# Kernel tuning notes

Measured on AMD Instinct MI355X. Metric: run time of the kernel, lower is better.

## Reference

```python
import jax, jax.numpy as jnp
import numpy as np

E = 160000      # num edges
N = 10000       # num nodes
M1 = 16         # rep1.mult
M2 = 8          # rep2.mult (output)
D1 = 3          # rep1.dim
D2 = 3          # rep2.dim
NREPS = 2       # repr.nreps()
EDGE_DIM = 32
HID = 64
NHEADS = 4
HIDDEN_SIZE = M2 * D2            # 24, attention hidden size
HEAD_DIM = HIDDEN_SIZE // NHEADS # 6
M2H = 3 * M2                     # repr_h.rep2.mult = 24 (k,q,v fused)
TMP_OUT = NREPS * M1 * M2H       # 768, RadialWeight layer2 out dim


def setup_inputs() -> dict:
    key = jax.random.key(0)
    ks = jax.random.split(key, 9)
    src = jax.random.randint(ks[0], (E,), 0, N)
    dst = jax.random.randint(ks[1], (E,), 0, N)
    basis = jax.random.normal(ks[2], (E, D1, NREPS * D2), dtype=jnp.float32)
    edge_feats = jax.random.normal(ks[3], (E, EDGE_DIM), dtype=jnp.float32)
    f = jax.random.normal(ks[4], (N, M1, D1), dtype=jnp.float32)
    W1 = jax.random.normal(ks[5], (HID, EDGE_DIM), dtype=jnp.float32) * 0.05
    b1 = jnp.zeros((HID,), dtype=jnp.float32)
    W2 = jax.random.normal(ks[6], (TMP_OUT, HID), dtype=jnp.float32) * 0.05
    b2 = jnp.zeros((TMP_OUT,), dtype=jnp.float32)
    return {"src": src, "dst": dst, "basis": basis, "edge_feats": edge_feats,
            "f": f, "W1": W1, "b1": b1, "W2": W2, "b2": b2}


def reference(src, dst, basis, edge_feats, f, W1, b1, W2, b2):
    # --- RadialWeight: 2-layer MLP on invariant edge feats ---
    h = jax.nn.relu(edge_feats @ W1.T + b1)               # (E, HID)
    rw = (h @ W2.T + b2).reshape(E, M2H, M1 * NREPS)      # (E, 3*m2, m1*nreps)

    # --- Equivariant convolution: gather by src, basis matmul, radial mix ---
    fe = f[src]                                           # (E, m1, d1)
    tmp = jnp.einsum('emd,edk->emk', fe, basis)           # (E, m1, nreps*d2)
    tmp = tmp.reshape(E, M1 * NREPS, D2)                  # (E, m1*nreps, d2)
    conv = jnp.einsum('ecm,emd->ecd', rw, tmp)            # (E, 3*m2, d2)

    # --- split into k, q, v along the multiplicity (feature) dim ---
    k, q, v = jnp.split(conv, 3, axis=1)                  # each (E, m2, d2)
    k = k.reshape(E, NHEADS, HEAD_DIM)
    q = q.reshape(E, NHEADS, HEAD_DIM)
    v = v.reshape(E, NHEADS, HEAD_DIM)

    # --- graph attention: LeakyReLU scores + edge softmax over dst ---
    temp = HIDDEN_SIZE ** (-0.5)
    scores = jnp.sum(k * q, axis=-1) * temp               # (E, NHEADS)
    scores = jax.nn.leaky_relu(scores, negative_slope=0.2)
    smax = jax.ops.segment_max(scores, dst, num_segments=N)   # (N, NHEADS)
    ex = jnp.exp(scores - smax[dst])                      # (E, NHEADS)
    denom = jax.ops.segment_sum(ex, dst, num_segments=N)  # (N, NHEADS)
    weights = ex / denom[dst]                             # (E, NHEADS)

    # --- weighted values, scatter-sum to dst nodes ---
    wv = weights[..., None] * v                           # (E, NHEADS, HEAD_DIM)
    out = jax.ops.segment_sum(wv, dst, num_segments=N)    # (N, NHEADS, HEAD_DIM)
    return out.reshape(N, M2, D2)
```

## Files before the change

### kernel.cpp

```cpp
#include <hip/hip_runtime.h>

#define E_EDGES 160000
#define N_NODES 10000
#define SLOTS   32

#define TEMP 0.20412414523193154f

typedef __fp16 half2_t __attribute__((ext_vector_type(2)));
typedef __fp16 half8_t __attribute__((ext_vector_type(8)));
typedef float f32x4 __attribute__((ext_vector_type(4)));

__device__ __forceinline__ float fdot2(half2_t a, half2_t b, float c) {
#if __has_builtin(__builtin_amdgcn_fdot2)
    return __builtin_amdgcn_fdot2(a, b, c, false);
#else
    return fmaf((float)a.x, (float)b.x, fmaf((float)a.y, (float)b.y, c));
#endif
}
__device__ __forceinline__ half2_t pk(float a, float b) {
    return __builtin_amdgcn_cvt_pkrtz(a, b);
}

__global__ __launch_bounds__(256)
void prep_kernel(const float* __restrict__ W2, const float* __restrict__ W1,
                 unsigned* __restrict__ w2p, uint4* __restrict__ w1pk,
                 int* __restrict__ cnt, float4* __restrict__ zbuf)
{
    int u = blockIdx.x * blockDim.x + threadIdx.x;
    if (u < N_NODES) cnt[u] = 0;
    #pragma unroll
    for (int i = 0; i < 3; ++i) {
        int z = u + i * 24576;
        if (z < (N_NODES * 28) / 4) zbuf[z] = make_float4(0.f, 0.f, 0.f, 0.f);
    }
    if (u < 256) {
        int t = u >> 6, l = u & 63;
        int r16 = l & 15, q = l >> 4;
        int row = 32*(t >> 1) + ((r16 >> 2) << 3) + ((t & 1) << 2) + (r16 & 3);
        union { __fp16 h[8]; uint4 v; } o2;
        #pragma unroll
        for (int i = 0; i < 8; ++i) o2.h[i] = (__fp16)W1[row*32 + q*8 + i];
        w1pk[(t << 6) + l] = o2.v;
    }
    int tp    = u & 3;
    int lane  = (u >> 2) & 63;
    int piece = (u >> 8) & 3;
    int c     = u >> 10;
    int em = lane & 15, quad = lane >> 4;
    int row = 32*c + ((piece >> 1) << 4) + em;
    int col = ((piece & 1) << 5) + quad*8 + 2*tp;
    union { half2_t h; unsigned v; } o;
    o.h.x = (__fp16)W2[row*64 + col];
    o.h.y = (__fp16)W2[row*64 + col + 1];
    w2p[u] = o.v;
}

#define CONV_GROUP(GBASE, cbase, OUT) \
    _Pragma("unroll") \
    for (int cg = 0; cg < 8; ++cg) { \
        const int c = (cbase) + cg; \
        const uint4* wg = (GBASE) + cg*256 + lane; \
        union { uint4 u; half8_t v; } u0, u1, u2, u3; \
        u0.u = wg[0]; u1.u = wg[64]; u2.u = wg[128]; u3.u = wg[192]; \
        half8_t wa0 = u0.v, wa1 = u1.v, wb0 = u2.v, wb1 = u3.v; \
        float4 bb0 = *(const float4*)(b2s + 32*c + quad*4); \
        float4 bb1 = *(const float4*)(b2s + 32*c + 16 + quad*4); \
        f32x4 acc0 = {bb0.x, bb0.y, bb0.z, bb0.w}; \
        acc0 = __builtin_amdgcn_mfma_f32_16x16x32_f16(wa0, h_lo, acc0, 0, 0, 0); \
        acc0 = __builtin_amdgcn_mfma_f32_16x16x32_f16(wa1, h_hi, acc0, 0, 0, 0); \
        f32x4 acc1 = {bb1.x, bb1.y, bb1.z, bb1.w}; \
        acc1 = __builtin_amdgcn_mfma_f32_16x16x32_f16(wb0, h_lo, acc1, 0, 0, 0); \
        acc1 = __builtin_amdgcn_mfma_f32_16x16x32_f16(wb1, h_hi, acc1, 0, 0, 0); \
        float p0 = 0.f, p1 = 0.f, p2 = 0.f; \
        _Pragma("unroll") \
        for (int r = 0; r < 4; ++r) { \
            half2_t rp = pk(acc0[r], acc1[r]); \
            p0 = fdot2(rp, t2[r][0], p0); \
            p1 = fdot2(rp, t2[r][1], p1); \
            p2 = fdot2(rp, t2[r][2], p2); \
        } \
        p0 += __shfl_xor(p0, 16); p0 += __shfl_xor(p0, 32); \
        p1 += __shfl_xor(p1, 16); p1 += __shfl_xor(p1, 32); \
        p2 += __shfl_xor(p2, 16); p2 += __shfl_xor(p2, 32); \
        OUT; \
    }

__global__ __launch_bounds__(256, 2)
void fused_kernel(const int* __restrict__ src, const int* __restrict__ dst,
                  const float* __restrict__ basis, const float* __restrict__ efeat,
                  const float* __restrict__ f,
                  const uint4* __restrict__ w1pk, const float* __restrict__ b1,
                  const uint4* __restrict__ w2p, const float* __restrict__ b2,
                  unsigned char* __restrict__ bkt, int* __restrict__ cnt,
                  float* __restrict__ num, float* __restrict__ den)
{
    __shared__ float b2s[768];

    const int tid  = threadIdx.x;
    const int lane = tid & 63;
    const int wid  = tid >> 6;
    const int em   = lane & 15;
    const int quad = lane >> 4;
    const int e = (blockIdx.x * 4 + wid) * 16 + em;

    if (tid < 192) ((float4*)b2s)[tid] = ((const float4*)b2)[tid];

    half8_t w1f[4];
    {
        #pragma unroll
        for (int t = 0; t < 4; ++t) {
            union { uint4 u; half8_t v; } c;
            c.u = w1pk[(t << 6) + lane];
            w1f[t] = c.v;
        }
    }
    float4 b1a = *(const float4*)(b1 + quad*8);
    float4 b1b = *(const float4*)(b1 + quad*8 + 4);
    float4 b1c = *(const float4*)(b1 + 32 + quad*8);
    float4 b1d = *(const float4*)(b1 + 32 + quad*8 + 4);

    half8_t xb;
    {
        const float4* xv = (const float4*)(efeat + (size_t)e * 32 + quad*8);
        float4 x0 = xv[0], x1 = xv[1];
        union { half2_t h2[4]; half8_t v; } xu;
        xu.h2[0] = pk(x0.x, x0.y); xu.h2[1] = pk(x0.z, x0.w);
        xu.h2[2] = pk(x1.x, x1.y); xu.h2[3] = pk(x1.z, x1.w);
        xb = xu.v;
    }

    int p_slot = 0, dn0 = 0;
    if (quad == 0) {
        dn0 = dst[e];
        p_slot = atomicAdd(&cnt[dn0], 1);
    }
    const int pb  = __shfl(p_slot, em);
    const int dnb = __shfl(dn0, em);

    half8_t h_lo, h_hi;
    {
        f32x4 ha0 = {b1a.x, b1a.y, b1a.z, b1a.w};
        f32x4 ha1 = {b1b.x, b1b.y, b1b.z, b1b.w};
        f32x4 ha2 = {b1c.x, b1c.y, b1c.z, b1c.w};
        f32x4 ha3 = {b1d.x, b1d.y, b1d.z, b1d.w};
        ha0 = __builtin_amdgcn_mfma_f32_16x16x32_f16(w1f[0], xb, ha0, 0, 0, 0);
        ha1 = __builtin_amdgcn_mfma_f32_16x16x32_f16(w1f[1], xb, ha1, 0, 0, 0);
        ha2 = __builtin_amdgcn_mfma_f32_16x16x32_f16(w1f[2], xb, ha2, 0, 0, 0);
        ha3 = __builtin_amdgcn_mfma_f32_16x16x32_f16(w1f[3], xb, ha3, 0, 0, 0);
        union { half2_t h2[4]; half8_t v; } lo, hi;
        lo.h2[0] = pk(fmaxf(ha0[0],0.f), fmaxf(ha0[1],0.f));
        lo.h2[1] = pk(fmaxf(ha0[2],0.f), fmaxf(ha0[3],0.f));
        lo.h2[2] = pk(fmaxf(ha1[0],0.f), fmaxf(ha1[1],0.f));
        lo.h2[3] = pk(fmaxf(ha1[2],0.f), fmaxf(ha1[3],0.f));
        hi.h2[0] = pk(fmaxf(ha2[0],0.f), fmaxf(ha2[1],0.f));
        hi.h2[1] = pk(fmaxf(ha2[2],0.f), fmaxf(ha2[3],0.f));
        hi.h2[2] = pk(fmaxf(ha3[0],0.f), fmaxf(ha3[1],0.f));
        hi.h2[3] = pk(fmaxf(ha3[2],0.f), fmaxf(ha3[3],0.f));
        h_lo = lo.v; h_hi = hi.v;
    }

    half2_t t2[4][3];
    {
        float bas[18];
        const float2* bv = (const float2*)(basis + (size_t)e * 18);
        #pragma unroll
        for (int i = 0; i < 9; ++i) { float2 t = bv[i]; bas[2*i] = t.x; bas[2*i+1] = t.y; }
        const float* fp = f + (size_t)src[e] * 48 + quad*6;
        float fl[6], fh[6];
        #pragma unroll
        for (int i = 0; i < 3; ++i) {
            float2 a = *(const float2*)(fp + 2*i);      fl[2*i] = a.x; fl[2*i+1] = a.y;
            float2 b = *(const float2*)(fp + 24 + 2*i); fh[2*i] = b.x; fh[2*i+1] = b.y;
        }
        #pragma unroll
        for (int jj = 0; jj < 4; ++jj) {
            const int mr = (jj >> 1) * 3;
            const int rb = (jj & 1) * 3;
            #pragma unroll
            for (int d = 0; d < 3; ++d) {
                float lo = fmaf(fl[mr+0], bas[rb+d],
                           fmaf(fl[mr+1], bas[6+rb+d], fl[mr+2] * bas[12+rb+d]));
                float hi = fmaf(fh[mr+0], bas[rb+d],
                           fmaf(fh[mr+1], bas[6+rb+d], fh[mr+2] * bas[12+rb+d]));
                t2[jj][d] = pk(lo, hi);
            }
        }
    }

    __syncthreads();

    float kreg[8][3];
    CONV_GROUP(w2p, 0, { kreg[cg][0]=p0; kreg[cg][1]=p1; kreg[cg][2]=p2; });

    float sreg[4];
    CONV_GROUP(w2p + 2048, 8, {
        float s_ = p0*kreg[cg][0] + p1*kreg[cg][1] + p2*kreg[cg][2];
        if ((cg & 1) == 0) sreg[cg>>1] = s_; else sreg[cg>>1] += s_;
    });

    float exv[4];
    #pragma unroll
    for (int hh = 0; hh < 4; ++hh) {
        float s = sreg[hh] * TEMP;
        s = (s > 0.0f) ? s : 0.2f * s;
        exv[hh] = __expf(s);
    }

    float vreg[8][3];
    CONV_GROUP(w2p + 4096, 16, { vreg[cg][0]=p0; vreg[cg][1]=p1; vreg[cg][2]=p2; });

    if (pb < SLOTS) {
        unsigned char* rec = bkt + ((size_t)dnb * SLOTS + pb) * 64;
        if (quad == 3) {
            *(float4*)(rec + 48) = make_float4(exv[0], exv[1], exv[2], exv[3]);
        } else {
            union { half2_t h2[4]; uint4 u; } pv;
            if (quad == 0) {
                pv.h2[0] = pk(vreg[0][0], vreg[0][1]);
                pv.h2[1] = pk(vreg[0][2], vreg[1][0]);
                pv.h2[2] = pk(vreg[1][1], vreg[1][2]);
                pv.h2[3] = pk(vreg[2][0], vreg[2][1]);
            } else if (quad == 1) {
                pv.h2[0] = pk(vreg[2][2], vreg[3][0]);
                pv.h2[1] = pk(vreg[3][1], vreg[3][2]);
                pv.h2[2] = pk(vreg[4][0], vreg[4][1]);
                pv.h2[3] = pk(vreg[4][2], vreg[5][0]);
            } else {
                pv.h2[0] = pk(vreg[5][1], vreg[5][2]);
                pv.h2[1] = pk(vreg[6][0], vreg[6][1]);
                pv.h2[2] = pk(vreg[6][2], vreg[7][0]);
                pv.h2[3] = pk(vreg[7][1], vreg[7][2]);
            }
            *(uint4*)(rec + quad*16) = pv.u;
        }
    } else {
        float* nb = num + (size_t)dnb * 24;
        if (quad == 0) {
            atomicAdd(nb+0, exv[0]*vreg[0][0]); atomicAdd(nb+1, exv[0]*vreg[0][1]);
            atomicAdd(nb+2, exv[0]*vreg[0][2]); atomicAdd(nb+3, exv[0]*vreg[1][0]);
            atomicAdd(nb+4, exv[0]*vreg[1][1]); atomicAdd(nb+5, exv[0]*vreg[1][2]);
            atomicAdd(nb+6, exv[1]*vreg[2][0]); atomicAdd(nb+7, exv[1]*vreg[2][1]);
        } else if (quad == 1) {
            atomicAdd(nb+8,  exv[1]*vreg[2][2]); atomicAdd(nb+9,  exv[1]*vreg[3][0]);
            atomicAdd(nb+10, exv[1]*vreg[3][1]); atomicAdd(nb+11, exv[1]*vreg[3][2]);
            atomicAdd(nb+12, exv[2]*vreg[4][0]); atomicAdd(nb+13, exv[2]*vreg[4][1]);
            atomicAdd(nb+14, exv[2]*vreg[4][2]); atomicAdd(nb+15, exv[2]*vreg[5][0]);
        } else if (quad == 2) {
            atomicAdd(nb+16, exv[2]*vreg[5][1]); atomicAdd(nb+17, exv[2]*vreg[5][2]);
            atomicAdd(nb+18, exv[3]*vreg[6][0]); atomicAdd(nb+19, exv[3]*vreg[6][1]);
            atomicAdd(nb+20, exv[3]*vreg[6][2]); atomicAdd(nb+21, exv[3]*vreg[7][0]);
            atomicAdd(nb+22, exv[3]*vreg[7][1]); atomicAdd(nb+23, exv[3]*vreg[7][2]);
        } else {
            float* db = den + (size_t)dnb * 4;
            atomicAdd(db+0, exv[0]); atomicAdd(db+1, exv[1]);
            atomicAdd(db+2, exv[2]); atomicAdd(db+3, exv[3]);
        }
    }
}

__global__ __launch_bounds__(256)
void gather_kernel(const int* __restrict__ cnt, const unsigned char* __restrict__ bkt,
                   const float* __restrict__ num, const float* __restrict__ den,
                   float* __restrict__ out)
{
    const int lane = threadIdx.x & 63;
    const int wid  = threadIdx.x >> 6;
    const int n = blockIdx.x * 4 + wid;
    if (n >= N_NODES) return;
    int deg = cnt[n];
    if (deg > SLOTS) deg = SLOTS;
    const unsigned char* rec = bkt + (size_t)n * SLOTS * 64;

    const int j = lane & 31;
    const int half = lane >> 5;
    const int hd = (j < 24) ? (j / 6) : 0;

    float acc = 0.f, dn_ = 0.f;
    if (j < 24 && half == 0) {
        acc = num[n*24 + j];
        dn_ = den[n*4 + hd];
    }
    if (j < 24) {
        #pragma unroll 2
        for (int i = half; i < deg; i += 2) {
            const unsigned char* r = rec + (size_t)i * 64;
            float ex = *(const float*)(r + 48 + hd*4);
            float v  = (float)*(const __fp16*)(r + j*2);
            dn_ += ex;
            acc = fmaf(ex, v, acc);
        }
    }
    acc += __shfl_xor(acc, 32);
    dn_ += __shfl_xor(dn_, 32);
    if (half == 0 && j < 24) {
        out[n*24 + j] = (dn_ > 0.f) ? (acc / dn_) : 0.f;
    }
}

extern "C" void kernel_launch(void* const* d_in, const int* in_sizes, int n_in,
                              void* d_out, int out_size, void* d_ws, size_t ws_size,
                              hipStream_t stream)
{
    const int*   src   = (const int*)d_in[0];
    const int*   dst   = (const int*)d_in[1];
    const float* basis = (const float*)d_in[2];
    const float* ef    = (const float*)d_in[3];
    const float* f     = (const float*)d_in[4];
    const float* W1    = (const float*)d_in[5];
    const float* b1    = (const float*)d_in[6];
    const float* W2    = (const float*)d_in[7];
    const float* b2    = (const float*)d_in[8];
    float* out = (float*)d_out;

    unsigned char* bkt = (unsigned char*)d_ws;
    float* num = (float*)(bkt + (size_t)N_NODES * SLOTS * 64);
    float* den = num + (size_t)N_NODES * 24;
    unsigned* w2p = (unsigned*)(den + (size_t)N_NODES * 4);
    int* cnt = (int*)(w2p + 24576);
    uint4* w1pk = (uint4*)(cnt + N_NODES);

    prep_kernel<<<96, 256, 0, stream>>>(W2, W1, w2p, w1pk, cnt, (float4*)num);

    fused_kernel<<<E_EDGES / 64, 256, 0, stream>>>(src, dst, basis, ef, f,
                                                   w1pk, b1, (const uint4*)w2p, b2,
                                                   bkt, cnt, num, den);

    gather_kernel<<<(N_NODES + 3) / 4, 256, 0, stream>>>(cnt, bkt, num, den, out);
}
```

Baseline: 155.3 us.

## Stage W2 fragments in LDS and process two edge tiles per wave

Each wave now handles 32 edges (two 16-edge tiles) instead of 16, and the block stages the packed W2 weights for the k and q parts into shared memory, later reloading the v part into the same buffer. Weight fragments are loaded once per cg and reused for both edge tiles, which halves global and L2 weight traffic per edge and halves the grid size. In exchange the kernel uses about 64KB of LDS plus extra barriers and roughly double the live registers, so occupancy may drop under the launch bound of 2 blocks per SM.

```diff
diff --git a/kernel.cpp b/kernel.cpp
--- a/kernel.cpp
+++ b/kernel.cpp
@@ -55,35 +55,123 @@
     w2p[u] = o.v;
 }
 
-#define CONV_GROUP(GBASE, cbase, OUT) \
+#define MFMA4_TAIL(F0,F1,F2,F3,HL,HH,BB0,BB1,T2,P0,P1,P2) { \
+    f32x4 a0 = {(BB0).x, (BB0).y, (BB0).z, (BB0).w}; \
+    a0 = __builtin_amdgcn_mfma_f32_16x16x32_f16((F0), (HL), a0, 0, 0, 0); \
+    a0 = __builtin_amdgcn_mfma_f32_16x16x32_f16((F1), (HH), a0, 0, 0, 0); \
+    f32x4 a1 = {(BB1).x, (BB1).y, (BB1).z, (BB1).w}; \
+    a1 = __builtin_amdgcn_mfma_f32_16x16x32_f16((F2), (HL), a1, 0, 0, 0); \
+    a1 = __builtin_amdgcn_mfma_f32_16x16x32_f16((F3), (HH), a1, 0, 0, 0); \
+    P0 = 0.f; P1 = 0.f; P2 = 0.f; \
     _Pragma("unroll") \
-    for (int cg = 0; cg < 8; ++cg) { \
-        const int c = (cbase) + cg; \
-        const uint4* wg = (GBASE) + cg*256 + lane; \
-        union { uint4 u; half8_t v; } u0, u1, u2, u3; \
-        u0.u = wg[0]; u1.u = wg[64]; u2.u = wg[128]; u3.u = wg[192]; \
-        half8_t wa0 = u0.v, wa1 = u1.v, wb0 = u2.v, wb1 = u3.v; \
-        float4 bb0 = *(const float4*)(b2s + 32*c + quad*4); \
-        float4 bb1 = *(const float4*)(b2s + 32*c + 16 + quad*4); \
-        f32x4 acc0 = {bb0.x, bb0.y, bb0.z, bb0.w}; \
-        acc0 = __builtin_amdgcn_mfma_f32_16x16x32_f16(wa0, h_lo, acc0, 0, 0, 0); \
-        acc0 = __builtin_amdgcn_mfma_f32_16x16x32_f16(wa1, h_hi, acc0, 0, 0, 0); \
-        f32x4 acc1 = {bb1.x, bb1.y, bb1.z, bb1.w}; \
-        acc1 = __builtin_amdgcn_mfma_f32_16x16x32_f16(wb0, h_lo, acc1, 0, 0, 0); \
-        acc1 = __builtin_amdgcn_mfma_f32_16x16x32_f16(wb1, h_hi, acc1, 0, 0, 0); \
-        float p0 = 0.f, p1 = 0.f, p2 = 0.f; \
+    for (int r = 0; r < 4; ++r) { \
+        half2_t rp = pk(a0[r], a1[r]); \
+        P0 = fdot2(rp, (T2)[r][0], P0); \
+        P1 = fdot2(rp, (T2)[r][1], P1); \
+        P2 = fdot2(rp, (T2)[r][2], P2); \
+    } \
+    P0 += __shfl_xor(P0, 16); P0 += __shfl_xor(P0, 32); \
+    P1 += __shfl_xor(P1, 16); P1 += __shfl_xor(P1, 32); \
+    P2 += __shfl_xor(P2, 16); P2 += __shfl_xor(P2, 32); \
+}
+
+#define PHASE_A(XB, HLO, HHI) { \
+    f32x4 ha0 = {b1a.x, b1a.y, b1a.z, b1a.w}; \
+    f32x4 ha1 = {b1b.x, b1b.y, b1b.z, b1b.w}; \
+    f32x4 ha2 = {b1c.x, b1c.y, b1c.z, b1c.w}; \
+    f32x4 ha3 = {b1d.x, b1d.y, b1d.z, b1d.w}; \
+    ha0 = __builtin_amdgcn_mfma_f32_16x16x32_f16(w1f[0], (XB), ha0, 0, 0, 0); \
+    ha1 = __builtin_amdgcn_mfma_f32_16x16x32_f16(w1f[1], (XB), ha1, 0, 0, 0); \
+    ha2 = __builtin_amdgcn_mfma_f32_16x16x32_f16(w1f[2], (XB), ha2, 0, 0, 0); \
+    ha3 = __builtin_amdgcn_mfma_f32_16x16x32_f16(w1f[3], (XB), ha3, 0, 0, 0); \
+    union { half2_t h2[4]; half8_t v; } lo, hi; \
+    lo.h2[0] = pk(fmaxf(ha0[0],0.f), fmaxf(ha0[1],0.f)); \
+    lo.h2[1] = pk(fmaxf(ha0[2],0.f), fmaxf(ha0[3],0.f)); \
+    lo.h2[2] = pk(fmaxf(ha1[0],0.f), fmaxf(ha1[1],0.f)); \
+    lo.h2[3] = pk(fmaxf(ha1[2],0.f), fmaxf(ha1[3],0.f)); \
+    hi.h2[0] = pk(fmaxf(ha2[0],0.f), fmaxf(ha2[1],0.f)); \
+    hi.h2[1] = pk(fmaxf(ha2[2],0.f), fmaxf(ha2[3],0.f)); \
+    hi.h2[2] = pk(fmaxf(ha3[0],0.f), fmaxf(ha3[1],0.f)); \
+    hi.h2[3] = pk(fmaxf(ha3[2],0.f), fmaxf(ha3[3],0.f)); \
+    (HLO) = lo.v; (HHI) = hi.v; \
+}
+
+#define PHASE_B(E, T2OUT) { \
+    float bas[18]; \
+    const float2* bv = (const float2*)(basis + (size_t)(E) * 18); \
+    _Pragma("unroll") \
+    for (int i = 0; i < 9; ++i) { float2 t = bv[i]; bas[2*i] = t.x; bas[2*i+1] = t.y; } \
+    const float* fp = f + (size_t)src[(E)] * 48 + quad*6; \
+    float fl[6], fh[6]; \
+    _Pragma("unroll") \
+    for (int i = 0; i < 3; ++i) { \
+        float2 a = *(const float2*)(fp + 2*i);      fl[2*i] = a.x; fl[2*i+1] = a.y; \
+        float2 b = *(const float2*)(fp + 24 + 2*i); fh[2*i] = b.x; fh[2*i+1] = b.y; \
+    } \
+    _Pragma("unroll") \
+    for (int jj = 0; jj < 4; ++jj) { \
+        const int mr = (jj >> 1) * 3; \
+        const int rb = (jj & 1) * 3; \
         _Pragma("unroll") \
-        for (int r = 0; r < 4; ++r) { \
-            half2_t rp = pk(acc0[r], acc1[r]); \
-            p0 = fdot2(rp, t2[r][0], p0); \
-            p1 = fdot2(rp, t2[r][1], p1); \
-            p2 = fdot2(rp, t2[r][2], p2); \
+        for (int d = 0; d < 3; ++d) { \
+            float lo = fmaf(fl[mr+0], bas[rb+d], \
+                       fmaf(fl[mr+1], bas[6+rb+d], fl[mr+2] * bas[12+rb+d])); \
+            float hi = fmaf(fh[mr+0], bas[rb+d], \
+                       fmaf(fh[mr+1], bas[6+rb+d], fh[mr+2] * bas[12+rb+d])); \
+            (T2OUT)[jj][d] = pk(lo, hi); \
         } \
-        p0 += __shfl_xor(p0, 16); p0 += __shfl_xor(p0, 32); \
-        p1 += __shfl_xor(p1, 16); p1 += __shfl_xor(p1, 32); \
-        p2 += __shfl_xor(p2, 16); p2 += __shfl_xor(p2, 32); \
-        OUT; \
-    }
+    } \
+}
+
+#define EPILOGUE(PB, DNB, VREG, EXV) { \
+    if ((PB) < SLOTS) { \
+        unsigned char* rec = bkt + ((size_t)(DNB) * SLOTS + (PB)) * 64; \
+        if (quad == 3) { \
+            *(float4*)(rec + 48) = make_float4((EXV)[0], (EXV)[1], (EXV)[2], (EXV)[3]); \
+        } else { \
+            union { half2_t h2[4]; uint4 u; } pv; \
+            if (quad == 0) { \
+                pv.h2[0] = pk((VREG)[0][0], (VREG)[0][1]); \
+                pv.h2[1] = pk((VREG)[0][2], (VREG)[1][0]); \
+                pv.h2[2] = pk((VREG)[1][1], (VREG)[1][2]); \
+                pv.h2[3] = pk((VREG)[2][0], (VREG)[2][1]); \
+            } else if (quad == 1) { \
+                pv.h2[0] = pk((VREG)[2][2], (VREG)[3][0]); \
+                pv.h2[1] = pk((VREG)[3][1], (VREG)[3][2]); \
+                pv.h2[2] = pk((VREG)[4][0], (VREG)[4][1]); \
+                pv.h2[3] = pk((VREG)[4][2], (VREG)[5][0]); \
+            } else { \
+                pv.h2[0] = pk((VREG)[5][1], (VREG)[5][2]); \
+                pv.h2[1] = pk((VREG)[6][0], (VREG)[6][1]); \
+                pv.h2[2] = pk((VREG)[6][2], (VREG)[7][0]); \
+                pv.h2[3] = pk((VREG)[7][1], (VREG)[7][2]); \
+            } \
+            *(uint4*)(rec + quad*16) = pv.u; \
+        } \
+    } else { \
+        float* nb = num + (size_t)(DNB) * 24; \
+        if (quad == 0) { \
+            atomicAdd(nb+0, (EXV)[0]*(VREG)[0][0]); atomicAdd(nb+1, (EXV)[0]*(VREG)[0][1]); \
+            atomicAdd(nb+2, (EXV)[0]*(VREG)[0][2]); atomicAdd(nb+3, (EXV)[0]*(VREG)[1][0]); \
+            atomicAdd(nb+4, (EXV)[0]*(VREG)[1][1]); atomicAdd(nb+5, (EXV)[0]*(VREG)[1][2]); \
+            atomicAdd(nb+6, (EXV)[1]*(VREG)[2][0]); atomicAdd(nb+7, (EXV)[1]*(VREG)[2][1]); \
+        } else if (quad == 1) { \
+            atomicAdd(nb+8,  (EXV)[1]*(VREG)[2][2]); atomicAdd(nb+9,  (EXV)[1]*(VREG)[3][0]); \
+            atomicAdd(nb+10, (EXV)[1]*(VREG)[3][1]); atomicAdd(nb+11, (EXV)[1]*(VREG)[3][2]); \
+            atomicAdd(nb+12, (EXV)[2]*(VREG)[4][0]); atomicAdd(nb+13, (EXV)[2]*(VREG)[4][1]); \
+            atomicAdd(nb+14, (EXV)[2]*(VREG)[4][2]); atomicAdd(nb+15, (EXV)[2]*(VREG)[5][0]); \
+        } else if (quad == 2) { \
+            atomicAdd(nb+16, (EXV)[2]*(VREG)[5][1]); atomicAdd(nb+17, (EXV)[2]*(VREG)[5][2]); \
+            atomicAdd(nb+18, (EXV)[3]*(VREG)[6][0]); atomicAdd(nb+19, (EXV)[3]*(VREG)[6][1]); \
+            atomicAdd(nb+20, (EXV)[3]*(VREG)[6][2]); atomicAdd(nb+21, (EXV)[3]*(VREG)[7][0]); \
+            atomicAdd(nb+22, (EXV)[3]*(VREG)[7][1]); atomicAdd(nb+23, (EXV)[3]*(VREG)[7][2]); \
+        } else { \
+            float* db = den + (size_t)(DNB) * 4; \
+            atomicAdd(db+0, (EXV)[0]); atomicAdd(db+1, (EXV)[1]); \
+            atomicAdd(db+2, (EXV)[2]); atomicAdd(db+3, (EXV)[3]); \
+        } \
+    } \
+}
 
 __global__ __launch_bounds__(256, 2)
 void fused_kernel(const int* __restrict__ src, const int* __restrict__ dst,
@@ -94,167 +182,157 @@
                   unsigned char* __restrict__ bkt, int* __restrict__ cnt,
                   float* __restrict__ num, float* __restrict__ den)
 {
-    __shared__ float b2s[768];
+    __shared__ __fp16 w2s[2*16384];
+    __shared__ float  b2s[768];
 
     const int tid  = threadIdx.x;
     const int lane = tid & 63;
     const int wid  = tid >> 6;
     const int em   = lane & 15;
     const int quad = lane >> 4;
-    const int e = (blockIdx.x * 4 + wid) * 16 + em;
-
-    if (tid < 192) ((float4*)b2s)[tid] = ((const float4*)b2)[tid];
+    const int base = (blockIdx.x * 4 + wid) * 32;
+    const int e0 = base + em;
+    const int e1 = base + 16 + em;
+
+    {
+        uint4* d4 = (uint4*)w2s;
+        #pragma unroll
+        for (int i = 0; i < 8; ++i) d4[i*256 + tid] = w2p[i*256 + tid];
+        #pragma unroll
+        for (int i = 0; i < 8; ++i) d4[2048 + i*256 + tid] = w2p[2048 + i*256 + tid];
+        if (tid < 192) ((float4*)b2s)[tid] = ((const float4*)b2)[tid];
+    }
+
+    int p_slot = 0, dn0 = 0;
+    if (quad == 0) {
+        dn0 = dst[e0];
+        p_slot = atomicAdd(&cnt[dn0], 1);
+    } else if (quad == 1) {
+        dn0 = dst[e1];
+        p_slot = atomicAdd(&cnt[dn0], 1);
+    }
+    const int pb0  = __shfl(p_slot, em);
+    const int dnb0 = __shfl(dn0, em);
+    const int pb1  = __shfl(p_slot, 16 + em);
+    const int dnb1 = __shfl(dn0, 16 + em);
 
     half8_t w1f[4];
-    {
-        #pragma unroll
-        for (int t = 0; t < 4; ++t) {
-            union { uint4 u; half8_t v; } c;
-            c.u = w1pk[(t << 6) + lane];
-            w1f[t] = c.v;
-        }
+    #pragma unroll
+    for (int t = 0; t < 4; ++t) {
+        union { uint4 u; half8_t v; } c;
+        c.u = w1pk[(t << 6) + lane];
+        w1f[t] = c.v;
     }
     float4 b1a = *(const float4*)(b1 + quad*8);
     float4 b1b = *(const float4*)(b1 + quad*8 + 4);
     float4 b1c = *(const float4*)(b1 + 32 + quad*8);
     float4 b1d = *(const float4*)(b1 + 32 + quad*8 + 4);
 
-    half8_t xb;
+    half8_t xb0, xb1;
     {
-        const float4* xv = (const float4*)(efeat + (size_t)e * 32 + quad*8);
+        const float4* xv = (const float4*)(efeat + (size_t)e0 * 32 + quad*8);
         float4 x0 = xv[0], x1 = xv[1];
         union { half2_t h2[4]; half8_t v; } xu;
         xu.h2[0] = pk(x0.x, x0.y); xu.h2[1] = pk(x0.z, x0.w);
         xu.h2[2] = pk(x1.x, x1.y); xu.h2[3] = pk(x1.z, x1.w);
-        xb = xu.v;
-    }
-
-    int p_slot = 0, dn0 = 0;
-    if (quad == 0) {
-        dn0 = dst[e];
-        p_slot = atomicAdd(&cnt[dn0], 1);
-    }
-    const int pb  = __shfl(p_slot, em);
-    const int dnb = __shfl(dn0, em);
-
-    half8_t h_lo, h_hi;
-    {
-        f32x4 ha0 = {b1a.x, b1a.y, b1a.z, b1a.w};
-        f32x4 ha1 = {b1b.x, b1b.y, b1b.z, b1b.w};
-        f32x4 ha2 = {b1c.x, b1c.y, b1c.z, b1c.w};
-        f32x4 ha3 = {b1d.x, b1d.y, b1d.z, b1d.w};
-        ha0 = __builtin_amdgcn_mfma_f32_16x16x32_f16(w1f[0], xb, ha0, 0, 0, 0);
-        ha1 = __builtin_amdgcn_mfma_f32_16x16x32_f16(w1f[1], xb, ha1, 0, 0, 0);
-        ha2 = __builtin_amdgcn_mfma_f32_16x16x32_f16(w1f[2], xb, ha2, 0, 0, 0);
-        ha3 = __builtin_amdgcn_mfma_f32_16x16x32_f16(w1f[3], xb, ha3, 0, 0, 0);
-        union { half2_t h2[4]; half8_t v; } lo, hi;
-        lo.h2[0] = pk(fmaxf(ha0[0],0.f), fmaxf(ha0[1],0.f));
-        lo.h2[1] = pk(fmaxf(ha0[2],0.f), fmaxf(ha0[3],0.f));
-        lo.h2[2] = pk(fmaxf(ha1[0],0.f), fmaxf(ha1[1],0.f));
-        lo.h2[3] = pk(fmaxf(ha1[2],0.f), fmaxf(ha1[3],0.f));
-        hi.h2[0] = pk(fmaxf(ha2[0],0.f), fmaxf(ha2[1],0.f));
-        hi.h2[1] = pk(fmaxf(ha2[2],0.f), fmaxf(ha2[3],0.f));
-        hi.h2[2] = pk(fmaxf(ha3[0],0.f), fmaxf(ha3[1],0.f));
-        hi.h2[3] = pk(fmaxf(ha3[2],0.f), fmaxf(ha3[3],0.f));
-        h_lo = lo.v; h_hi = hi.v;
-    }
-
-    half2_t t2[4][3];
-    {
-        float bas[18];
-        const float2* bv = (const float2*)(basis + (size_t)e * 18);
-        #pragma unroll
-        for (int i = 0; i < 9; ++i) { float2 t = bv[i]; bas[2*i] = t.x; bas[2*i+1] = t.y; }
-        const float* fp = f + (size_t)src[e] * 48 + quad*6;
-        float fl[6], fh[6];
-        #pragma unroll
-        for (int i = 0; i < 3; ++i) {
-            float2 a = *(const float2*)(fp + 2*i);      fl[2*i] = a.x; fl[2*i+1] = a.y;
-            float2 b = *(const float2*)(fp + 24 + 2*i); fh[2*i] = b.x; fh[2*i+1] = b.y;
-        }
-        #pragma unroll
-        for (int jj = 0; jj < 4; ++jj) {
-            const int mr = (jj >> 1) * 3;
-            const int rb = (jj & 1) * 3;
-            #pragma unroll
-            for (int d = 0; d < 3; ++d) {
-                float lo = fmaf(fl[mr+0], bas[rb+d],
-                           fmaf(fl[mr+1], bas[6+rb+d], fl[mr+2] * bas[12+rb+d]));
-                float hi = fmaf(fh[mr+0], bas[rb+d],
-                           fmaf(fh[mr+1], bas[6+rb+d], fh[mr+2] * bas[12+rb+d]));
-                t2[jj][d] = pk(lo, hi);
-            }
-        }
-    }
+        xb0 = xu.v;
+        const float4* yv = (const float4*)(efeat + (size_t)e1 * 32 + quad*8);
+        float4 y0 = yv[0], y1 = yv[1];
+        xu.h2[0] = pk(y0.x, y0.y); xu.h2[1] = pk(y0.z, y0.w);
+        xu.h2[2] = pk(y1.x, y1.y); xu.h2[3] = pk(y1.z, y1.w);
+        xb1 = xu.v;
+    }
+
+    half8_t h_lo0, h_hi0, h_lo1, h_hi1;
+    PHASE_A(xb0, h_lo0, h_hi0);
+    PHASE_A(xb1, h_lo1, h_hi1);
+
+    half2_t t20[4][3], t21[4][3];
+    PHASE_B(e0, t20);
+    PHASE_B(e1, t21);
 
     __syncthreads();
 
-    float kreg[8][3];
-    CONV_GROUP(w2p, 0, { kreg[cg][0]=p0; kreg[cg][1]=p1; kreg[cg][2]=p2; });
-
-    float sreg[4];
-    CONV_GROUP(w2p + 2048, 8, {
-        float s_ = p0*kreg[cg][0] + p1*kreg[cg][1] + p2*kreg[cg][2];
-        if ((cg & 1) == 0) sreg[cg>>1] = s_; else sreg[cg>>1] += s_;
-    });
-
-    float exv[4];
+    float sreg0[4], sreg1[4];
+    #pragma unroll
+    for (int cg = 0; cg < 8; ++cg) {
+        const __fp16* kp = w2s + ((cg*4)*64 + lane)*8;
+        half8_t kf0 = *(const half8_t*)(kp);
+        half8_t kf1 = *(const half8_t*)(kp + 512);
+        half8_t kf2 = *(const half8_t*)(kp + 1024);
+        half8_t kf3 = *(const half8_t*)(kp + 1536);
+        const __fp16* qp = kp + 16384;
+        half8_t qf0 = *(const half8_t*)(qp);
+        half8_t qf1 = *(const half8_t*)(qp + 512);
+        half8_t qf2 = *(const half8_t*)(qp + 1024);
+        half8_t qf3 = *(const half8_t*)(qp + 1536);
+        float4 bk0 = *(const float4*)(b2s + 32*cg + quad*4);
+        float4 bk1 = *(const float4*)(b2s + 32*cg + 16 + quad*4);
+        float4 bq0 = *(const float4*)(b2s + 32*(8+cg) + quad*4);
+        float4 bq1 = *(const float4*)(b2s + 32*(8+cg) + 16 + quad*4);
+        float k0, k1, k2, q0, q1, q2, s_;
+        MFMA4_TAIL(kf0,kf1,kf2,kf3, h_lo0,h_hi0, bk0,bk1, t20, k0,k1,k2);
+        MFMA4_TAIL(qf0,qf1,qf2,qf3, h_lo0,h_hi0, bq0,bq1, t20, q0,q1,q2);
+        s_ = q0*k0 + q1*k1 + q2*k2;
+        if ((cg & 1) == 0) sreg0[cg>>1] = s_; else sreg0[cg>>1] += s_;
+        MFMA4_TAIL(kf0,kf1,kf2,kf3, h_lo1,h_hi1, bk0,bk1, t21, k0,k1,k2);
+        MFMA4_TAIL(qf0,qf1,qf2,qf3, h_lo1,h_hi1, bq0,bq1, t21, q0,q1,q2);
+        s_ = q0*k0 + q1*k1 + q2*k2;
+        if ((cg & 1) == 0) sreg1[cg>>1] = s_; else sreg1[cg>>1] += s_;
+    }
+
+    float exv0[4], exv1[4];
     #pragma unroll
     for (int hh = 0; hh < 4; ++hh) {
-        float s = sreg[hh] * TEMP;
+        float s = sreg0[hh] * TEMP;
         s = (s > 0.0f) ? s : 0.2f * s;
-        exv[hh] = __expf(s);
-    }
-
-    float vreg[8][3];
-    CONV_GROUP(w2p + 4096, 16, { vreg[cg][0]=p0; vreg[cg][1]=p1; vreg[cg][2]=p2; });
-
-    if (pb < SLOTS) {
-        unsigned char* rec = bkt + ((size_t)dnb * SLOTS + pb) * 64;
-        if (quad == 3) {
-            *(float4*)(rec + 48) = make_float4(exv[0], exv[1], exv[2], exv[3]);
-        } else {
-            union { half2_t h2[4]; uint4 u; } pv;
-            if (quad == 0) {
-                pv.h2[0] = pk(vreg[0][0], vreg[0][1]);
-                pv.h2[1] = pk(vreg[0][2], vreg[1][0]);
-                pv.h2[2] = pk(vreg[1][1], vreg[1][2]);
-                pv.h2[3] = pk(vreg[2][0], vreg[2][1]);
-            } else if (quad == 1) {
-                pv.h2[0] = pk(vreg[2][2], vreg[3][0]);
-                pv.h2[1] = pk(vreg[3][1], vreg[3][2]);
-                pv.h2[2] = pk(vreg[4][0], vreg[4][1]);
-                pv.h2[3] = pk(vreg[4][2], vreg[5][0]);
-            } else {
-                pv.h2[0] = pk(vreg[5][1], vreg[5][2]);
-                pv.h2[1] = pk(vreg[6][0], vreg[6][1]);
-                pv.h2[2] = pk(vreg[6][2], vreg[7][0]);
-                pv.h2[3] = pk(vreg[7][1], vreg[7][2]);
-            }
-            *(uint4*)(rec + quad*16) = pv.u;
+        exv0[hh] = __expf(s);
+        float t = sreg1[hh] * TEMP;
+        t = (t > 0.0f) ? t : 0.2f * t;
+        exv1[hh] = __expf(t);
+    }
+
+    __syncthreads();
+
+    {
+        uint4* d4 = (uint4*)w2s;
+        #pragma unroll
+        for (int i = 0; i < 8; ++i) d4[i*256 + tid] = w2p[4096 + i*256 + tid];
+    }
+
+    __syncthreads();
+
+    {
+        float vreg[8][3];
+        #pragma unroll
+        for (int cg = 0; cg < 8; ++cg) {
+            const __fp16* vp = w2s + ((cg*4)*64 + lane)*8;
+            half8_t vf0 = *(const half8_t*)(vp);
+            half8_t vf1 = *(const half8_t*)(vp + 512);
+            half8_t vf2 = *(const half8_t*)(vp + 1024);
+            half8_t vf3 = *(const half8_t*)(vp + 1536);
+            float4 bv0 = *(const float4*)(b2s + 32*(16+cg) + quad*4);
+            float4 bv1 = *(const float4*)(b2s + 32*(16+cg) + 16 + quad*4);
+            MFMA4_TAIL(vf0,vf1,vf2,vf3, h_lo0,h_hi0, bv0,bv1, t20,
+                       vreg[cg][0], vreg[cg][1], vreg[cg][2]);
         }
-    } else {
-        float* nb = num + (size_t)dnb * 24;
-        if (quad == 0) {
-            atomicAdd(nb+0, exv[0]*vreg[0][0]); atomicAdd(nb+1, exv[0]*vreg[0][1]);
-            atomicAdd(nb+2, exv[0]*vreg[0][2]); atomicAdd(nb+3, exv[0]*vreg[1][0]);
-            atomicAdd(nb+4, exv[0]*vreg[1][1]); atomicAdd(nb+5, exv[0]*vreg[1][2]);
-            atomicAdd(nb+6, exv[1]*vreg[2][0]); atomicAdd(nb+7, exv[1]*vreg[2][1]);
-        } else if (quad == 1) {
-            atomicAdd(nb+8,  exv[1]*vreg[2][2]); atomicAdd(nb+9,  exv[1]*vreg[3][0]);
-            atomicAdd(nb+10, exv[1]*vreg[3][1]); atomicAdd(nb+11, exv[1]*vreg[3][2]);
-            atomicAdd(nb+12, exv[2]*vreg[4][0]); atomicAdd(nb+13, exv[2]*vreg[4][1]);
-            atomicAdd(nb+14, exv[2]*vreg[4][2]); atomicAdd(nb+15, exv[2]*vreg[5][0]);
-        } else if (quad == 2) {
-            atomicAdd(nb+16, exv[2]*vreg[5][1]); atomicAdd(nb+17, exv[2]*vreg[5][2]);
-            atomicAdd(nb+18, exv[3]*vreg[6][0]); atomicAdd(nb+19, exv[3]*vreg[6][1]);
-            atomicAdd(nb+20, exv[3]*vreg[6][2]); atomicAdd(nb+21, exv[3]*vreg[7][0]);
-            atomicAdd(nb+22, exv[3]*vreg[7][1]); atomicAdd(nb+23, exv[3]*vreg[7][2]);
-        } else {
-            float* db = den + (size_t)dnb * 4;
-            atomicAdd(db+0, exv[0]); atomicAdd(db+1, exv[1]);
-            atomicAdd(db+2, exv[2]); atomicAdd(db+3, exv[3]);
+        EPILOGUE(pb0, dnb0, vreg, exv0);
+    }
+    {
+        float vreg[8][3];
+        #pragma unroll
+        for (int cg = 0; cg < 8; ++cg) {
+            const __fp16* vp = w2s + ((cg*4)*64 + lane)*8;
+            half8_t vf0 = *(const half8_t*)(vp);
+            half8_t vf1 = *(const half8_t*)(vp + 512);
+            half8_t vf2 = *(const half8_t*)(vp + 1024);
+            half8_t vf3 = *(const half8_t*)(vp + 1536);
+            float4 bv0 = *(const float4*)(b2s + 32*(16+cg) + quad*4);
+            float4 bv1 = *(const float4*)(b2s + 32*(16+cg) + 16 + quad*4);
+            MFMA4_TAIL(vf0,vf1,vf2,vf3, h_lo1,h_hi1, bv0,bv1, t21,
+                       vreg[cg][0], vreg[cg][1], vreg[cg][2]);
         }
+        EPILOGUE(pb1, dnb1, vreg, exv1);
     }
 }
 
@@ -321,9 +399,9 @@
 
     prep_kernel<<<96, 256, 0, stream>>>(W2, W1, w2p, w1pk, cnt, (float4*)num);
 
-    fused_kernel<<<E_EDGES / 64, 256, 0, stream>>>(src, dst, basis, ef, f,
-                                                   w1pk, b1, (const uint4*)w2p, b2,
-                                                   bkt, cnt, num, den);
+    fused_kernel<<<E_EDGES / 128, 256, 0, stream>>>(src, dst, basis, ef, f,
+                                                    w1pk, b1, (const uint4*)w2p, b2,
+                                                    bkt, cnt, num, den);
 
     gather_kernel<<<(N_NODES + 3) / 4, 256, 0, stream>>>(cnt, bkt, num, den, out);
 }
```

Result: no change. 155.7 us (+0.2%).

## Stage W2 fragments in LDS and interleave k/q conv to drop kreg

Applied to the files above, without the earlier changes.

Each block now copies the packed fp16 W2 fragments for k and q (64 KB) into shared memory, and later reloads the v portion into the same buffer between barriers. MFMA operands come from LDS instead of per-wave global/L2 loads. The k and q convolutions are computed together per group, so the 24-float kreg array disappears, and launch bounds rise to 3 blocks per CU. The dst atomic slot claim is also moved earlier. In exchange, every block pays a large cooperative copy plus two extra barriers, and 64 KB of LDS per block may cap occupancy below the requested 3 blocks.

```diff
diff --git a/kernel.cpp b/kernel.cpp
--- a/kernel.cpp
+++ b/kernel.cpp
@@ -55,37 +55,27 @@
     w2p[u] = o.v;
 }
 
-#define CONV_GROUP(GBASE, cbase, OUT) \
+#define MFMA4_TAIL(F0,F1,F2,F3,HL,HH,BB0,BB1,T2,P0,P1,P2) { \
+    f32x4 a0 = {(BB0).x, (BB0).y, (BB0).z, (BB0).w}; \
+    a0 = __builtin_amdgcn_mfma_f32_16x16x32_f16((F0), (HL), a0, 0, 0, 0); \
+    a0 = __builtin_amdgcn_mfma_f32_16x16x32_f16((F1), (HH), a0, 0, 0, 0); \
+    f32x4 a1 = {(BB1).x, (BB1).y, (BB1).z, (BB1).w}; \
+    a1 = __builtin_amdgcn_mfma_f32_16x16x32_f16((F2), (HL), a1, 0, 0, 0); \
+    a1 = __builtin_amdgcn_mfma_f32_16x16x32_f16((F3), (HH), a1, 0, 0, 0); \
+    P0 = 0.f; P1 = 0.f; P2 = 0.f; \
     _Pragma("unroll") \
-    for (int cg = 0; cg < 8; ++cg) { \
-        const int c = (cbase) + cg; \
-        const uint4* wg = (GBASE) + cg*256 + lane; \
-        union { uint4 u; half8_t v; } u0, u1, u2, u3; \
-        u0.u = wg[0]; u1.u = wg[64]; u2.u = wg[128]; u3.u = wg[192]; \
-        half8_t wa0 = u0.v, wa1 = u1.v, wb0 = u2.v, wb1 = u3.v; \
-        float4 bb0 = *(const float4*)(b2s + 32*c + quad*4); \
-        float4 bb1 = *(const float4*)(b2s + 32*c + 16 + quad*4); \
-        f32x4 acc0 = {bb0.x, bb0.y, bb0.z, bb0.w}; \
-        acc0 = __builtin_amdgcn_mfma_f32_16x16x32_f16(wa0, h_lo, acc0, 0, 0, 0); \
-        acc0 = __builtin_amdgcn_mfma_f32_16x16x32_f16(wa1, h_hi, acc0, 0, 0, 0); \
-        f32x4 acc1 = {bb1.x, bb1.y, bb1.z, bb1.w}; \
-        acc1 = __builtin_amdgcn_mfma_f32_16x16x32_f16(wb0, h_lo, acc1, 0, 0, 0); \
-        acc1 = __builtin_amdgcn_mfma_f32_16x16x32_f16(wb1, h_hi, acc1, 0, 0, 0); \
-        float p0 = 0.f, p1 = 0.f, p2 = 0.f; \
-        _Pragma("unroll") \
-        for (int r = 0; r < 4; ++r) { \
-            half2_t rp = pk(acc0[r], acc1[r]); \
-            p0 = fdot2(rp, t2[r][0], p0); \
-            p1 = fdot2(rp, t2[r][1], p1); \
-            p2 = fdot2(rp, t2[r][2], p2); \
-        } \
-        p0 += __shfl_xor(p0, 16); p0 += __shfl_xor(p0, 32); \
-        p1 += __shfl_xor(p1, 16); p1 += __shfl_xor(p1, 32); \
-        p2 += __shfl_xor(p2, 16); p2 += __shfl_xor(p2, 32); \
-        OUT; \
-    }
-
-__global__ __launch_bounds__(256, 2)
+    for (int r = 0; r < 4; ++r) { \
+        half2_t rp = pk(a0[r], a1[r]); \
+        P0 = fdot2(rp, (T2)[r][0], P0); \
+        P1 = fdot2(rp, (T2)[r][1], P1); \
+        P2 = fdot2(rp, (T2)[r][2], P2); \
+    } \
+    P0 += __shfl_xor(P0, 16); P0 += __shfl_xor(P0, 32); \
+    P1 += __shfl_xor(P1, 16); P1 += __shfl_xor(P1, 32); \
+    P2 += __shfl_xor(P2, 16); P2 += __shfl_xor(P2, 32); \
+}
+
+__global__ __launch_bounds__(256, 3)
 void fused_kernel(const int* __restrict__ src, const int* __restrict__ dst,
                   const float* __restrict__ basis, const float* __restrict__ efeat,
                   const float* __restrict__ f,
@@ -94,7 +84,8 @@
                   unsigned char* __restrict__ bkt, int* __restrict__ cnt,
                   float* __restrict__ num, float* __restrict__ den)
 {
-    __shared__ float b2s[768];
+    __shared__ __fp16 w2s[2*16384];
+    __shared__ float  b2s[768];
 
     const int tid  = threadIdx.x;
     const int lane = tid & 63;
@@ -103,16 +94,27 @@
     const int quad = lane >> 4;
     const int e = (blockIdx.x * 4 + wid) * 16 + em;
 
-    if (tid < 192) ((float4*)b2s)[tid] = ((const float4*)b2)[tid];
+    {
+        uint4* d4 = (uint4*)w2s;
+        #pragma unroll
+        for (int i = 0; i < 16; ++i) d4[i*256 + tid] = w2p[i*256 + tid];
+        if (tid < 192) ((float4*)b2s)[tid] = ((const float4*)b2)[tid];
+    }
+
+    int p_slot = 0, dn0 = 0;
+    if (quad == 0) {
+        dn0 = dst[e];
+        p_slot = atomicAdd(&cnt[dn0], 1);
+    }
+    const int pb  = __shfl(p_slot, em);
+    const int dnb = __shfl(dn0, em);
 
     half8_t w1f[4];
-    {
-        #pragma unroll
-        for (int t = 0; t < 4; ++t) {
-            union { uint4 u; half8_t v; } c;
-            c.u = w1pk[(t << 6) + lane];
-            w1f[t] = c.v;
-        }
+    #pragma unroll
+    for (int t = 0; t < 4; ++t) {
+        union { uint4 u; half8_t v; } c;
+        c.u = w1pk[(t << 6) + lane];
+        w1f[t] = c.v;
     }
     float4 b1a = *(const float4*)(b1 + quad*8);
     float4 b1b = *(const float4*)(b1 + quad*8 + 4);
@@ -128,14 +130,6 @@
         xu.h2[2] = pk(x1.x, x1.y); xu.h2[3] = pk(x1.z, x1.w);
         xb = xu.v;
     }
-
-    int p_slot = 0, dn0 = 0;
-    if (quad == 0) {
-        dn0 = dst[e];
-        p_slot = atomicAdd(&cnt[dn0], 1);
-    }
-    const int pb  = __shfl(p_slot, em);
-    const int dnb = __shfl(dn0, em);
 
     half8_t h_lo, h_hi;
     {
@@ -189,14 +183,29 @@
 
     __syncthreads();
 
-    float kreg[8][3];
-    CONV_GROUP(w2p, 0, { kreg[cg][0]=p0; kreg[cg][1]=p1; kreg[cg][2]=p2; });
-
     float sreg[4];
-    CONV_GROUP(w2p + 2048, 8, {
-        float s_ = p0*kreg[cg][0] + p1*kreg[cg][1] + p2*kreg[cg][2];
+    #pragma unroll
+    for (int cg = 0; cg < 8; ++cg) {
+        const __fp16* kp = w2s + ((cg*4)*64 + lane)*8;
+        half8_t kf0 = *(const half8_t*)(kp);
+        half8_t kf1 = *(const half8_t*)(kp + 512);
+        half8_t kf2 = *(const half8_t*)(kp + 1024);
+        half8_t kf3 = *(const half8_t*)(kp + 1536);
+        const __fp16* qp = kp + 16384;
+        half8_t qf0 = *(const half8_t*)(qp);
+        half8_t qf1 = *(const half8_t*)(qp + 512);
+        half8_t qf2 = *(const half8_t*)(qp + 1024);
+        half8_t qf3 = *(const half8_t*)(qp + 1536);
+        float4 bk0 = *(const float4*)(b2s + 32*cg + quad*4);
+        float4 bk1 = *(const float4*)(b2s + 32*cg + 16 + quad*4);
+        float4 bq0 = *(const float4*)(b2s + 32*(8+cg) + quad*4);
+        float4 bq1 = *(const float4*)(b2s + 32*(8+cg) + 16 + quad*4);
+        float k0, k1, k2, q0, q1, q2;
+        MFMA4_TAIL(kf0,kf1,kf2,kf3, h_lo,h_hi, bk0,bk1, t2, k0,k1,k2);
+        MFMA4_TAIL(qf0,qf1,qf2,qf3, h_lo,h_hi, bq0,bq1, t2, q0,q1,q2);
+        float s_ = q0*k0 + q1*k1 + q2*k2;
         if ((cg & 1) == 0) sreg[cg>>1] = s_; else sreg[cg>>1] += s_;
-    });
+    }
 
     float exv[4];
     #pragma unroll
@@ -206,8 +215,29 @@
         exv[hh] = __expf(s);
     }
 
+    __syncthreads();
+
+    {
+        uint4* d4 = (uint4*)w2s;
+        #pragma unroll
+        for (int i = 0; i < 8; ++i) d4[i*256 + tid] = w2p[4096 + i*256 + tid];
+    }
+
+    __syncthreads();
+
     float vreg[8][3];
-    CONV_GROUP(w2p + 4096, 16, { vreg[cg][0]=p0; vreg[cg][1]=p1; vreg[cg][2]=p2; });
+    #pragma unroll
+    for (int cg = 0; cg < 8; ++cg) {
+        const __fp16* vp = w2s + ((cg*4)*64 + lane)*8;
+        half8_t vf0 = *(const half8_t*)(vp);
+        half8_t vf1 = *(const half8_t*)(vp + 512);
+        half8_t vf2 = *(const half8_t*)(vp + 1024);
+        half8_t vf3 = *(const half8_t*)(vp + 1536);
+        float4 bv0 = *(const float4*)(b2s + 32*(16+cg) + quad*4);
+        float4 bv1 = *(const float4*)(b2s + 32*(16+cg) + 16 + quad*4);
+        MFMA4_TAIL(vf0,vf1,vf2,vf3, h_lo,h_hi, bv0,bv1, t2,
+                   vreg[cg][0], vreg[cg][1], vreg[cg][2]);
+    }
 
     if (pb < SLOTS) {
         unsigned char* rec = bkt + ((size_t)dnb * SLOTS + pb) * 64;
```

Result: slower. 158.6 us (+2.1%).
